# Kernel tuning notes

Measured on AMD Instinct MI355X. Metric: run time of the kernel, lower is better.

## Reference

```python
import jax, jax.numpy as jnp
import numpy as np

HEADS = 16
SEGS = 8


def _rotate_half(x):
    x1, x2 = jnp.split(x, 2, axis=-1)
    return jnp.concatenate([-x2, x1], axis=-1)


def _split_heads(t, h):
    b, n, dim = t.shape
    d = dim // h
    return t.reshape(b, n, h, d).transpose(0, 2, 1, 3).reshape(b * h, n, d)


def _merge_heads(t, b, h):
    c, n, d = t.shape
    return t.reshape(b, h, n, d).transpose(0, 2, 1, 3).reshape(b, n, h * d)


def setup_inputs() -> dict:
    key = jax.random.key(0)
    ks = jax.random.split(key, 5)
    b, n, dim = 2, 4096, 1024
    x = jax.random.normal(ks[0], (b, n, dim), dtype=jnp.float32)
    w = lambda k: jax.random.normal(k, (dim, dim), dtype=jnp.float32) * 0.02
    return {
        'x': x,
        'Wq': w(ks[1]),
        'Wkv': w(ks[2]),
        'Wo': w(ks[3]),
        'bo': jnp.zeros((dim,), jnp.float32),
        'Wo0': w(ks[4]),
        'bo0': jnp.zeros((dim,), jnp.float32),
    }


def reference(x, Wq, Wkv, Wo, bo, Wo0, bo0):
    b, n, dim = x.shape
    h = HEADS
    d = dim // h
    s = SEGS
    m = n // s  # segment_len
    mask_value = -jnp.finfo(x.dtype).max

    q = _split_heads(x @ Wq, h)    # (b*h, n, d)
    kv = _split_heads(x @ Wkv, h)  # (b*h, n, d)  (serves as both keys and values)

    # rotary embedding (layer_num == 0 branch)
    inv_freq = 1.0 / (10000.0 ** (jnp.arange(0, d, 2, dtype=jnp.float32) / d))
    freqs = jnp.arange(n, dtype=jnp.float32)[:, None] * inv_freq[None, :]  # (n, d/2)
    rot = jnp.concatenate([freqs, freqs], axis=-1)[None]  # (1, n, d)
    cos, sin = jnp.cos(rot), jnp.sin(rot)
    q = q * cos + _rotate_half(q) * sin
    kv = kv * cos + _rotate_half(kv) * sin

    q = q * (d ** -0.5)

    qs = q.reshape(-1, s, m, d)   # (c, s, m, d)
    kvs = kv.reshape(-1, s, m, d)

    # overlapping windows: segment t paired with segment t+1 as kv context
    kvs_ccs = jnp.concatenate([kvs[:, :-1], kvs[:, 1:]], axis=2)  # (c, s-1, 2m, d)
    qs_ccs = qs[:, 1:]                                            # (c, s-1, m, d)

    # NOTE: original computes lkv = LayerNorm(kvs_ccs) but never uses it (dead code) -> omitted.

    lsim = jnp.einsum('csmd,csnd->csmn', qs_ccs, kvs_ccs)  # (c, s-1, m, 2m)
    causal = jnp.triu(jnp.ones((m, m), dtype=bool), 1)
    # causal mask only applied to second half of keys (the own segment t+1)
    lsim = jnp.concatenate(
        [lsim[..., :m], jnp.where(causal, mask_value, lsim[..., m:])], axis=-1)

    attn0 = jnp.einsum('csmd,csnd->csmn', qs[:, :1], kvs[:, :1])  # (c, 1, m, m)
    attn0 = jnp.where(causal, mask_value, attn0)

    attn0 = jax.nn.softmax(attn0, axis=-1)
    attn1 = jax.nn.softmax(lsim, axis=-1)

    out0 = jnp.einsum('csij,csjd->csid', attn0, kvs[:, :1]).reshape(-1, m, d)
    out1 = jnp.einsum('csij,csjd->csid', attn1, kvs_ccs).reshape(-1, (s - 1) * m, d)

    out0 = _merge_heads(out0, b, h) @ Wo0 + bo0  # (b, m, dim)
    out1 = _merge_heads(out1, b, h) @ Wo + bo    # (b, (s-1)*m, dim)
    return jnp.concatenate([out0, out1], axis=1)  # (b, n, dim)
```

## Files before the change

kernel.cpp:

```cpp
#include <hip/hip_runtime.h>
#include <hip/hip_bf16.h>
#include <float.h>

using bf16 = __hip_bfloat16;
typedef __attribute__((ext_vector_type(8))) short bf16x8;
typedef __attribute__((ext_vector_type(4))) float f32x4;
typedef __attribute__((ext_vector_type(16))) float f32x16;

#define DIM   1024
#define NSEQ  4096
#define BATCH 2
#define NH    16
#define HD    64
#define NSEG  8
#define MSEG  512
#define ROWS  (BATCH*NSEQ)
#define NC    (BATCH*NH)
#define QSCALE (0.125f * 1.44269504f)

__device__ __forceinline__ float fast_exp2(float x) {
    float r;
    asm volatile("v_exp_f32 %0, %1" : "=v"(r) : "v"(x));
    return r;
}

__device__ __forceinline__ void gload16(const bf16* g, bf16* l) {
    __builtin_amdgcn_global_load_lds((const __attribute__((address_space(1))) unsigned int*)g,
                                     (__attribute__((address_space(3))) unsigned int*)l, 16, 0, 0);
}

__global__ void k_rope_tab(float* __restrict__ cosT, float* __restrict__ sinT) {
    int idx = blockIdx.x * 256 + threadIdx.x;
    int t = idx >> 5, i = idx & 31;
    float freq = 1.0f / powf(10000.0f, (float)(2 * i) * (1.0f / 64.0f));
    float a = (float)t * freq;
    cosT[idx] = cosf(a);
    sinT[idx] = sinf(a);
}

__global__ void k_convert_x(const float* __restrict__ X, bf16* __restrict__ Xb) {
    int i = (blockIdx.x * 256 + threadIdx.x) * 4;
    float4 v = *(const float4*)&X[i];
    union { bf16 h[4]; uint2 u; } p;
    p.h[0] = __float2bfloat16(v.x);
    p.h[1] = __float2bfloat16(v.y);
    p.h[2] = __float2bfloat16(v.z);
    p.h[3] = __float2bfloat16(v.w);
    *(uint2*)&Xb[i] = p.u;
}

__global__ void k_transpose(const float* __restrict__ W, bf16* __restrict__ Wt) {
    __shared__ float tile[32][33];
    int bx = blockIdx.x * 32;
    int by = blockIdx.y * 32;
    int tx = threadIdx.x;
    for (int i = threadIdx.y; i < 32; i += 8)
        tile[i][tx] = W[(size_t)(by + i) * DIM + bx + tx];
    __syncthreads();
    for (int i = threadIdx.y; i < 32; i += 8)
        Wt[(size_t)(bx + i) * DIM + by + tx] = __float2bfloat16(tile[tx][i]);
}

__launch_bounds__(256, 3)
__global__ void k_gemm_qkv(const bf16* __restrict__ A, const bf16* __restrict__ Bq,
                           const bf16* __restrict__ Bkv, const float* __restrict__ cosT,
                           const float* __restrict__ sinT, bf16* __restrict__ Qb,
                           bf16* __restrict__ KVf) {
    __shared__ alignas(16) bf16 SH[24576];
    bf16* AsB = SH;
    bf16* BsB = SH + 12288;
    const int K = DIM;
    int tid = threadIdx.x;
    int lane = tid & 63, wave = tid >> 6;
    int hi = lane >> 5, lq = lane & 31;
    int wr = (wave >> 1) * 64, wc = (wave & 1) * 64;
    int id = blockIdx.x;
    int xcd = id & 7, rank = id >> 3;
    int by = xcd * 8 + (rank >> 4);
    int bxx = rank & 15;
    int m0 = by * 128;
    bool isQ = (bxx < 8);
    const bf16* Bt = isQ ? Bq : Bkv;
    int n0 = (bxx & 7) * 128;
    int row = lane & 15, kk = (lane >> 4) * 8;
    int ch0 = wave * 128 + lane, ch1 = ch0 + 64;
    int r0 = ch0 >> 2, c0e = (ch0 & 3) * 8;
    int r1 = ch1 >> 2, c1e = (ch1 & 3) * 8;
    f32x4 acc[4][4] = {};

    auto stage = [&](int k0, int b) {
        gload16(&A[(size_t)(m0 + r0) * K + k0 + c0e], &AsB[b * 4096 + wave * 1024]);
        gload16(&A[(size_t)(m0 + r1) * K + k0 + c1e], &AsB[b * 4096 + wave * 1024 + 512]);
        gload16(&Bt[(size_t)(n0 + r0) * K + k0 + c0e], &BsB[b * 4096 + wave * 1024]);
        gload16(&Bt[(size_t)(n0 + r1) * K + k0 + c1e], &BsB[b * 4096 + wave * 1024 + 512]);
    };
    stage(0, 0);
    stage(32, 1);
    asm volatile("s_waitcnt vmcnt(4)" ::: "memory");
    __builtin_amdgcn_s_barrier();
    __builtin_amdgcn_sched_barrier(0);
    int cur = 0;
    for (int k = 0; k < 32; ++k) {
        if (k + 2 < 32) {
            int nb = cur + 2; if (nb >= 3) nb -= 3;
            stage(k * 32 + 64, nb);
        }
        bf16x8 af[4], bfr[4];
#pragma unroll
        for (int mt = 0; mt < 4; ++mt) af[mt] = *(const bf16x8*)&AsB[cur * 4096 + (wr + mt * 16 + row) * 32 + kk];
#pragma unroll
        for (int nt = 0; nt < 4; ++nt) bfr[nt] = *(const bf16x8*)&BsB[cur * 4096 + (wc + nt * 16 + row) * 32 + kk];
#pragma unroll
        for (int mt = 0; mt < 4; ++mt)
#pragma unroll
            for (int nt = 0; nt < 4; ++nt)
                acc[mt][nt] = __builtin_amdgcn_mfma_f32_16x16x32_bf16(af[mt], bfr[nt], acc[mt][nt], 0, 0, 0);
        if (k + 1 < 32) {
            if (k + 2 < 32) asm volatile("s_waitcnt vmcnt(4)" ::: "memory");
            else            asm volatile("s_waitcnt vmcnt(0)" ::: "memory");
            __builtin_amdgcn_s_barrier();
            __builtin_amdgcn_sched_barrier(0);
        }
        cur = cur + 1; if (cur == 3) cur = 0;
    }
    __syncthreads();
    bf16* Tw = SH + wave * (64 * 72);
    int orow = (lane >> 4) * 4, ocol = lane & 15;
    int head_g = (n0 + wc) >> 6;
    float sc = isQ ? QSCALE : 1.0f;
    int bidx = (m0 + wr) >> 12;
    int tbase = (m0 + wr) & (NSEQ - 1);
    int cch = bidx * NH + head_g;
#pragma unroll
    for (int mt = 0; mt < 4; ++mt) {
#pragma unroll
        for (int i = 0; i < 4; ++i) {
            int rl = mt * 16 + orow + i;
            int t = tbase + rl;
#pragma unroll
            for (int nt = 0; nt < 2; ++nt) {
                int e = nt * 16 + ocol;
                float x1 = acc[mt][nt][i], x2 = acc[mt][nt + 2][i];
                float cv = cosT[t * 32 + e], sv = sinT[t * 32 + e];
                Tw[rl * 72 + e]      = __float2bfloat16((x1 * cv - x2 * sv) * sc);
                Tw[rl * 72 + e + 32] = __float2bfloat16((x2 * cv + x1 * sv) * sc);
            }
        }
    }
    if (isQ) {
        int rsub = lane >> 3, dg = (lane & 7) * 8;
        size_t qbase = ((size_t)cch * NSEQ + tbase) * HD;
#pragma unroll
        for (int rr = 0; rr < 8; ++rr) {
            int rl = rr * 8 + rsub;
            *(uint4*)&Qb[qbase + (size_t)rl * HD + dg] = *(const uint4*)&Tw[rl * 72 + dg];
        }
    } else {
        size_t kvfbase = ((size_t)cch * 128 + (tbase >> 5)) * 4096;
#pragma unroll
        for (int st = 0; st < 2; ++st) {
            size_t tb = kvfbase + (size_t)st * 4096;
#pragma unroll
            for (int f = 0; f < 4; ++f)
                *(uint4*)&KVf[tb + f * 512 + lane * 8] =
                    *(const uint4*)&Tw[(st * 32 + lq) * 72 + f * 16 + hi * 8];
#pragma unroll
            for (int m = 0; m < 4; ++m) {
                int d0 = (m >> 1) * 32, sb = m & 1;
                union { bf16 h[8]; uint4 u; } pk;
#pragma unroll
                for (int j = 0; j < 8; ++j)
                    pk.h[j] = Tw[(st * 32 + sb * 16 + hi * 8 + j) * 72 + d0 + lq];
                *(uint4*)&KVf[tb + (size_t)(4 + m) * 512 + lane * 8] = pk.u;
            }
        }
    }
}

__launch_bounds__(256, 4)
__global__ void k_gemm_out(const bf16* __restrict__ A, const bf16* __restrict__ Bt0,
                           const bf16* __restrict__ Bt1, const float* __restrict__ bias0,
                           const float* __restrict__ bias1, float* __restrict__ C) {
    __shared__ alignas(16) bf16 As[3][128 * 32];
    __shared__ alignas(16) bf16 Bs[3][64 * 32];
    const int K = DIM;
    int tid = threadIdx.x;
    int lane = tid & 63, wave = tid >> 6;
    int wr = (wave >> 1) * 64, wc = (wave & 1) * 32;
    int id = blockIdx.x;
    int xcd = id & 7, rank = id >> 3;
    int by = xcd * 8 + (rank >> 4);
    int bx = rank & 15;
    int m0 = by * 128, n0 = bx * 64;
    bool first = (m0 & (NSEQ - 1)) < MSEG;
    const bf16* Bt = first ? Bt0 : Bt1;
    const float* bias = first ? bias0 : bias1;
    int row = lane & 15, kk = (lane >> 4) * 8;
    int ch0 = wave * 128 + lane, ch1 = ch0 + 64;
    int r0 = ch0 >> 2, c0e = (ch0 & 3) * 8;
    int r1 = ch1 >> 2, c1e = (ch1 & 3) * 8;
    int cb = wave * 64 + lane;
    int rb = cb >> 2, cbe = (cb & 3) * 8;
    f32x4 acc[4][2] = {};

    auto stage = [&](int k0, int b) {
        gload16(&A[(size_t)(m0 + r0) * K + k0 + c0e], &As[b][wave * 1024]);
        gload16(&A[(size_t)(m0 + r1) * K + k0 + c1e], &As[b][wave * 1024 + 512]);
        gload16(&Bt[(size_t)(n0 + rb) * K + k0 + cbe], &Bs[b][wave * 512]);
    };
    stage(0, 0);
    stage(32, 1);
    asm volatile("s_waitcnt vmcnt(3)" ::: "memory");
    __builtin_amdgcn_s_barrier();
    __builtin_amdgcn_sched_barrier(0);
    int cur = 0;
    for (int k = 0; k < 32; ++k) {
        if (k + 2 < 32) {
            int nb = cur + 2; if (nb >= 3) nb -= 3;
            stage(k * 32 + 64, nb);
        }
        bf16x8 af[4], bfr[2];
#pragma unroll
        for (int mt = 0; mt < 4; ++mt) af[mt] = *(const bf16x8*)&As[cur][(wr + mt * 16 + row) * 32 + kk];
#pragma unroll
        for (int nt = 0; nt < 2; ++nt) bfr[nt] = *(const bf16x8*)&Bs[cur][(wc + nt * 16 + row) * 32 + kk];
#pragma unroll
        for (int mt = 0; mt < 4; ++mt)
#pragma unroll
            for (int nt = 0; nt < 2; ++nt)
                acc[mt][nt] = __builtin_amdgcn_mfma_f32_16x16x32_bf16(af[mt], bfr[nt], acc[mt][nt], 0, 0, 0);
        if (k + 1 < 32) {
            if (k + 2 < 32) asm volatile("s_waitcnt vmcnt(3)" ::: "memory");
            else            asm volatile("s_waitcnt vmcnt(0)" ::: "memory");
            __builtin_amdgcn_s_barrier();
            __builtin_amdgcn_sched_barrier(0);
        }
        cur = cur + 1; if (cur == 3) cur = 0;
    }
    int orow = (lane >> 4) * 4, ocol = lane & 15;
#pragma unroll
    for (int mt = 0; mt < 4; ++mt)
#pragma unroll
        for (int nt = 0; nt < 2; ++nt) {
            float bv = bias[n0 + wc + nt * 16 + ocol];
#pragma unroll
            for (int i = 0; i < 4; ++i)
                C[(size_t)(m0 + wr + mt * 16 + orow + i) * DIM + n0 + wc + nt * 16 + ocol] = acc[mt][nt][i] + bv;
        }
}

__launch_bounds__(256, 4)
__global__ void k_attn(const bf16* __restrict__ Qb, const bf16* __restrict__ KVf,
                       bf16* __restrict__ Ob) {
    int lane = threadIdx.x & 63, wave = threadIdx.x >> 6;
    int hi = lane >> 5, lq = lane & 31;
    int id = blockIdx.x;
    int xcd = id & 7, rank = id >> 3;
    int c = xcd * 4 + (rank & 3);
    int hr = rank >> 2;
    int bx, seg;
    if (hr < 28) { bx = 3 - hr / 7; seg = 1 + hr % 7; }
    else         { seg = 0; bx = 31 - hr; }
    int i0 = bx * 128 + wave * 32;
    int bidx = c >> 4, head = c & 15;
    int tq = seg * MSEG + i0 + lq;
    const bf16* qptr = &Qb[((size_t)c * NSEQ + tq) * HD + hi * 8];
    bf16x8 qf[4];
#pragma unroll
    for (int dc = 0; dc < 4; ++dc) qf[dc] = *(const bf16x8*)&qptr[dc * 16];
    f32x16 o0 = {}, o1 = {};
    float mrun = -FLT_MAX, lrun = 0.f;
    int kvbase = (seg == 0) ? 0 : (seg - 1) * MSEG;
    int cstart = (seg == 0) ? 0 : MSEG;
    int cend = cstart + i0 + 32;
    int nT = cend >> 5;

    const bf16* fb = &KVf[((size_t)c * 128 + (kvbase >> 5)) * 4096 + lane * 8];

    bf16x8 ka0, ka1, ka2, ka3;
    f32x16 s;
    {
        bf16x8 k0 = *(const bf16x8*)&fb[0];
        bf16x8 k1 = *(const bf16x8*)&fb[512];
        bf16x8 k2 = *(const bf16x8*)&fb[1024];
        bf16x8 k3 = *(const bf16x8*)&fb[1536];
        if (nT > 1) {
            const bf16* p1 = fb + 4096;
            ka0 = *(const bf16x8*)&p1[0];
            ka1 = *(const bf16x8*)&p1[512];
            ka2 = *(const bf16x8*)&p1[1024];
            ka3 = *(const bf16x8*)&p1[1536];
        }
        f32x16 z = {};
        __builtin_amdgcn_s_setprio(1);
        z = __builtin_amdgcn_mfma_f32_32x32x16_bf16(k0, qf[0], z, 0, 0, 0);
        z = __builtin_amdgcn_mfma_f32_32x32x16_bf16(k1, qf[1], z, 0, 0, 0);
        z = __builtin_amdgcn_mfma_f32_32x32x16_bf16(k2, qf[2], z, 0, 0, 0);
        z = __builtin_amdgcn_mfma_f32_32x32x16_bf16(k3, qf[3], z, 0, 0, 0);
        __builtin_amdgcn_s_setprio(0);
        s = z;
    }

    for (int it = 0; it < nT; ++it) {
        int c0 = it * 32;
        const bf16* pv = fb + (size_t)it * 4096 + 2048;
        bf16x8 vf0 = *(const bf16x8*)&pv[0];
        bf16x8 vf1 = *(const bf16x8*)&pv[512];
        bf16x8 vf2 = *(const bf16x8*)&pv[1024];
        bf16x8 vf3 = *(const bf16x8*)&pv[1536];
        if (c0 + 31 >= cstart && c0 + 31 - cstart > i0) {
#pragma unroll
            for (int r = 0; r < 16; ++r) {
                int kvg = c0 + ((r & 3) + 8 * (r >> 2) + 4 * hi);
                if (kvg >= cstart && kvg - cstart > i0 + lq) s[r] = -FLT_MAX;
            }
        }
        float m8[8], m4[4];
#pragma unroll
        for (int r = 0; r < 8; ++r) m8[r] = fmaxf(s[2 * r], s[2 * r + 1]);
#pragma unroll
        for (int r = 0; r < 4; ++r) m4[r] = fmaxf(m8[2 * r], m8[2 * r + 1]);
        float vmax = fmaxf(fmaxf(m4[0], m4[1]), fmaxf(m4[2], m4[3]));
        vmax = fmaxf(vmax, __shfl_xor(vmax, 32));
        if (__any(vmax > mrun + 11.5f)) {
            float nm = fmaxf(mrun, vmax);
            float al = fast_exp2(mrun - nm);
#pragma unroll
            for (int r = 0; r < 16; ++r) { o0[r] *= al; o1[r] *= al; }
            lrun *= al;
            mrun = nm;
        }
        float p[16];
#pragma unroll
        for (int r = 0; r < 16; ++r) p[r] = fast_exp2(s[r] - mrun);
        if (it + 1 < nT) {
            f32x16 z = {};
            __builtin_amdgcn_s_setprio(1);
            z = __builtin_amdgcn_mfma_f32_32x32x16_bf16(ka0, qf[0], z, 0, 0, 0);
            z = __builtin_amdgcn_mfma_f32_32x32x16_bf16(ka1, qf[1], z, 0, 0, 0);
            z = __builtin_amdgcn_mfma_f32_32x32x16_bf16(ka2, qf[2], z, 0, 0, 0);
            z = __builtin_amdgcn_mfma_f32_32x32x16_bf16(ka3, qf[3], z, 0, 0, 0);
            __builtin_amdgcn_s_setprio(0);
            s = z;
            if (it + 2 < nT) {
                const bf16* pn = fb + (size_t)(it + 2) * 4096;
                ka0 = *(const bf16x8*)&pn[0];
                ka1 = *(const bf16x8*)&pn[512];
                ka2 = *(const bf16x8*)&pn[1024];
                ka3 = *(const bf16x8*)&pn[1536];
            }
        }
        float a8[8], a4[4];
#pragma unroll
        for (int r = 0; r < 8; ++r) a8[r] = p[2 * r] + p[2 * r + 1];
#pragma unroll
        for (int r = 0; r < 4; ++r) a4[r] = a8[2 * r] + a8[2 * r + 1];
        lrun += (a4[0] + a4[1]) + (a4[2] + a4[3]);
        unsigned pk[8];
#pragma unroll
        for (int k = 0; k < 8; ++k) {
            union { bf16 h[2]; unsigned u; } cv;
            cv.h[0] = __float2bfloat16(p[2 * k]);
            cv.h[1] = __float2bfloat16(p[2 * k + 1]);
            pk[k] = cv.u;
        }
        unsigned u0 = hi ? pk[0] : pk[2];
        unsigned u1 = hi ? pk[1] : pk[3];
        unsigned u2 = hi ? pk[4] : pk[6];
        unsigned u3 = hi ? pk[5] : pk[7];
        unsigned w0 = (unsigned)__shfl_xor((int)u0, 32);
        unsigned w1 = (unsigned)__shfl_xor((int)u1, 32);
        unsigned w2 = (unsigned)__shfl_xor((int)u2, 32);
        unsigned w3 = (unsigned)__shfl_xor((int)u3, 32);
        union { unsigned u[4]; bf16x8 v; } b0, b1;
        b0.u[0] = hi ? w0 : pk[0];
        b0.u[1] = hi ? w1 : pk[1];
        b0.u[2] = hi ? pk[2] : w0;
        b0.u[3] = hi ? pk[3] : w1;
        b1.u[0] = hi ? w2 : pk[4];
        b1.u[1] = hi ? w3 : pk[5];
        b1.u[2] = hi ? pk[6] : w2;
        b1.u[3] = hi ? pk[7] : w3;
        __builtin_amdgcn_s_setprio(1);
        o0 = __builtin_amdgcn_mfma_f32_32x32x16_bf16(vf0, b0.v, o0, 0, 0, 0);
        o1 = __builtin_amdgcn_mfma_f32_32x32x16_bf16(vf2, b0.v, o1, 0, 0, 0);
        o0 = __builtin_amdgcn_mfma_f32_32x32x16_bf16(vf1, b1.v, o0, 0, 0, 0);
        o1 = __builtin_amdgcn_mfma_f32_32x32x16_bf16(vf3, b1.v, o1, 0, 0, 0);
        __builtin_amdgcn_s_setprio(0);
    }
    lrun += __shfl_xor(lrun, 32);
    float inv = 1.0f / lrun;
    size_t obase = ((size_t)bidx * NSEQ + tq) * DIM + head * HD;
#pragma unroll
    for (int dt = 0; dt < 2; ++dt)
#pragma unroll
        for (int a = 0; a < 4; ++a) {
            union { bf16 h[4]; uint2 u; } pkd;
            const f32x16& ov = dt ? o1 : o0;
#pragma unroll
            for (int i = 0; i < 4; ++i) pkd.h[i] = __float2bfloat16(ov[4 * a + i] * inv);
            *(uint2*)&Ob[obase + dt * 32 + 8 * a + 4 * hi] = pkd.u;
        }
}

extern "C" void kernel_launch(void* const* d_in, const int* in_sizes, int n_in,
                              void* d_out, int out_size, void* d_ws, size_t ws_size,
                              hipStream_t stream) {
    const float* x   = (const float*)d_in[0];
    const float* Wq  = (const float*)d_in[1];
    const float* Wkv = (const float*)d_in[2];
    const float* Wo  = (const float*)d_in[3];
    const float* bo  = (const float*)d_in[4];
    const float* Wo0 = (const float*)d_in[5];
    const float* bo0 = (const float*)d_in[6];
    float* out = (float*)d_out;

    char* ws = (char*)d_ws;
    size_t off = 0;
    auto alloc = [&](size_t bytes) { void* p = ws + off; off += (bytes + 255) & ~(size_t)255; return p; };
    float* cosT = (float*)alloc((size_t)NSEQ * 32 * 4);
    float* sinT = (float*)alloc((size_t)NSEQ * 32 * 4);
    bf16* Xb    = (bf16*)alloc((size_t)ROWS * DIM * 2);
    bf16* WqT   = (bf16*)alloc((size_t)DIM * DIM * 2);
    bf16* WkvT  = (bf16*)alloc((size_t)DIM * DIM * 2);
    bf16* WoT   = (bf16*)alloc((size_t)DIM * DIM * 2);
    bf16* Wo0T  = (bf16*)alloc((size_t)DIM * DIM * 2);
    bf16* Qb    = (bf16*)alloc((size_t)NC * NSEQ * HD * 2);
    bf16* KVf   = (bf16*)alloc((size_t)NC * 128 * 4096 * 2);
    bf16* Ob    = (bf16*)alloc((size_t)ROWS * DIM * 2);

    hipLaunchKernelGGL(k_rope_tab, dim3(NSEQ * 32 / 256), dim3(256), 0, stream, cosT, sinT);
    hipLaunchKernelGGL(k_convert_x, dim3(ROWS * DIM / 4 / 256), dim3(256), 0, stream, x, Xb);
    hipLaunchKernelGGL(k_transpose, dim3(32, 32), dim3(32, 8), 0, stream, Wq, WqT);
    hipLaunchKernelGGL(k_transpose, dim3(32, 32), dim3(32, 8), 0, stream, Wkv, WkvT);
    hipLaunchKernelGGL(k_transpose, dim3(32, 32), dim3(32, 8), 0, stream, Wo, WoT);
    hipLaunchKernelGGL(k_transpose, dim3(32, 32), dim3(32, 8), 0, stream, Wo0, Wo0T);

    hipLaunchKernelGGL(k_gemm_qkv, dim3(1024), dim3(256), 0, stream, Xb, WqT, WkvT, cosT, sinT, Qb, KVf);

    hipLaunchKernelGGL(k_attn, dim3(1024), dim3(256), 0, stream, Qb, KVf, Ob);

    hipLaunchKernelGGL(k_gemm_out, dim3(1024), dim3(256), 0, stream, Ob, Wo0T, WoT, bo0, bo, out);
}
```

Measured before the change: 154.5 us.

## Merge prep kernels into one launch and XOR-swizzle GEMM LDS tiles

Six small preprocessing launches (rope table, x conversion, four weight transposes) become one kernel that picks its task from the block index, which removes launch gaps. Both GEMM kernels now XOR-swizzle the 8-element k-chunk column by row bits, both when staging global data into LDS and when reading MFMA fragments, to reduce LDS bank conflicts. The swizzle moves the permutation onto the global-load addresses, so each lane reads a permuted 16-byte chunk within its row.

New measurement: 142.6 us. -7.7%, faster.

```diff
diff --git a/kernel.cpp b/kernel.cpp
--- a/kernel.cpp
+++ b/kernel.cpp
@@ -29,36 +29,43 @@
                                      (__attribute__((address_space(3))) unsigned int*)l, 16, 0, 0);
 }
 
-__global__ void k_rope_tab(float* __restrict__ cosT, float* __restrict__ sinT) {
-    int idx = blockIdx.x * 256 + threadIdx.x;
-    int t = idx >> 5, i = idx & 31;
-    float freq = 1.0f / powf(10000.0f, (float)(2 * i) * (1.0f / 64.0f));
-    float a = (float)t * freq;
-    cosT[idx] = cosf(a);
-    sinT[idx] = sinf(a);
-}
-
-__global__ void k_convert_x(const float* __restrict__ X, bf16* __restrict__ Xb) {
-    int i = (blockIdx.x * 256 + threadIdx.x) * 4;
-    float4 v = *(const float4*)&X[i];
-    union { bf16 h[4]; uint2 u; } p;
-    p.h[0] = __float2bfloat16(v.x);
-    p.h[1] = __float2bfloat16(v.y);
-    p.h[2] = __float2bfloat16(v.z);
-    p.h[3] = __float2bfloat16(v.w);
-    *(uint2*)&Xb[i] = p.u;
-}
-
-__global__ void k_transpose(const float* __restrict__ W, bf16* __restrict__ Wt) {
+__global__ void k_prep(const float* __restrict__ x, bf16* __restrict__ Xb,
+                       const float* __restrict__ Wq, const float* __restrict__ Wkv,
+                       const float* __restrict__ Wo, const float* __restrict__ Wo0,
+                       bf16* __restrict__ WqT, bf16* __restrict__ WkvT,
+                       bf16* __restrict__ WoT, bf16* __restrict__ Wo0T,
+                       float* __restrict__ cosT, float* __restrict__ sinT) {
     __shared__ float tile[32][33];
-    int bx = blockIdx.x * 32;
-    int by = blockIdx.y * 32;
-    int tx = threadIdx.x;
-    for (int i = threadIdx.y; i < 32; i += 8)
-        tile[i][tx] = W[(size_t)(by + i) * DIM + bx + tx];
-    __syncthreads();
-    for (int i = threadIdx.y; i < 32; i += 8)
-        Wt[(size_t)(bx + i) * DIM + by + tx] = __float2bfloat16(tile[tx][i]);
+    int b = blockIdx.x, tid = threadIdx.x;
+    if (b < 8192) {
+        int i = (b * 256 + tid) * 4;
+        float4 v = *(const float4*)&x[i];
+        union { bf16 h[4]; uint2 u; } p;
+        p.h[0] = __float2bfloat16(v.x);
+        p.h[1] = __float2bfloat16(v.y);
+        p.h[2] = __float2bfloat16(v.z);
+        p.h[3] = __float2bfloat16(v.w);
+        *(uint2*)&Xb[i] = p.u;
+    } else if (b < 12288) {
+        int zz = (b - 8192) >> 10;
+        int bb = (b - 8192) & 1023;
+        int bxt = (bb & 31) * 32, byt = (bb >> 5) * 32;
+        const float* W = (zz == 0) ? Wq : (zz == 1) ? Wkv : (zz == 2) ? Wo : Wo0;
+        bf16* Wt = (zz == 0) ? WqT : (zz == 1) ? WkvT : (zz == 2) ? WoT : Wo0T;
+        int tx = tid & 31, ty = tid >> 5;
+        for (int ii = ty; ii < 32; ii += 8)
+            tile[ii][tx] = W[(size_t)(byt + ii) * DIM + bxt + tx];
+        __syncthreads();
+        for (int ii = ty; ii < 32; ii += 8)
+            Wt[(size_t)(bxt + ii) * DIM + byt + tx] = __float2bfloat16(tile[tx][ii]);
+    } else {
+        int idx = (b - 12288) * 256 + tid;
+        int t = idx >> 5, ii = idx & 31;
+        float freq = 1.0f / powf(10000.0f, (float)(2 * ii) * (1.0f / 64.0f));
+        float a = (float)t * freq;
+        cosT[idx] = cosf(a);
+        sinT[idx] = sinf(a);
+    }
 }
 
 __launch_bounds__(256, 3)
@@ -83,16 +90,19 @@
     const bf16* Bt = isQ ? Bq : Bkv;
     int n0 = (bxx & 7) * 128;
     int row = lane & 15, kk = (lane >> 4) * 8;
+    int kkA = kk ^ (((lane >> 1) & 3) << 3);
     int ch0 = wave * 128 + lane, ch1 = ch0 + 64;
     int r0 = ch0 >> 2, c0e = (ch0 & 3) * 8;
     int r1 = ch1 >> 2, c1e = (ch1 & 3) * 8;
+    int c0s = c0e ^ (((r0 >> 1) & 3) << 3);
+    int c1s = c1e ^ (((r1 >> 1) & 3) << 3);
     f32x4 acc[4][4] = {};
 
     auto stage = [&](int k0, int b) {
-        gload16(&A[(size_t)(m0 + r0) * K + k0 + c0e], &AsB[b * 4096 + wave * 1024]);
-        gload16(&A[(size_t)(m0 + r1) * K + k0 + c1e], &AsB[b * 4096 + wave * 1024 + 512]);
-        gload16(&Bt[(size_t)(n0 + r0) * K + k0 + c0e], &BsB[b * 4096 + wave * 1024]);
-        gload16(&Bt[(size_t)(n0 + r1) * K + k0 + c1e], &BsB[b * 4096 + wave * 1024 + 512]);
+        gload16(&A[(size_t)(m0 + r0) * K + k0 + c0s], &AsB[b * 4096 + wave * 1024]);
+        gload16(&A[(size_t)(m0 + r1) * K + k0 + c1s], &AsB[b * 4096 + wave * 1024 + 512]);
+        gload16(&Bt[(size_t)(n0 + r0) * K + k0 + c0s], &BsB[b * 4096 + wave * 1024]);
+        gload16(&Bt[(size_t)(n0 + r1) * K + k0 + c1s], &BsB[b * 4096 + wave * 1024 + 512]);
     };
     stage(0, 0);
     stage(32, 1);
@@ -107,9 +117,9 @@
         }
         bf16x8 af[4], bfr[4];
 #pragma unroll
-        for (int mt = 0; mt < 4; ++mt) af[mt] = *(const bf16x8*)&AsB[cur * 4096 + (wr + mt * 16 + row) * 32 + kk];
-#pragma unroll
-        for (int nt = 0; nt < 4; ++nt) bfr[nt] = *(const bf16x8*)&BsB[cur * 4096 + (wc + nt * 16 + row) * 32 + kk];
+        for (int mt = 0; mt < 4; ++mt) af[mt] = *(const bf16x8*)&AsB[cur * 4096 + (wr + mt * 16 + row) * 32 + kkA];
+#pragma unroll
+        for (int nt = 0; nt < 4; ++nt) bfr[nt] = *(const bf16x8*)&BsB[cur * 4096 + (wc + nt * 16 + row) * 32 + kkA];
 #pragma unroll
         for (int mt = 0; mt < 4; ++mt)
 #pragma unroll
@@ -196,17 +206,21 @@
     const bf16* Bt = first ? Bt0 : Bt1;
     const float* bias = first ? bias0 : bias1;
     int row = lane & 15, kk = (lane >> 4) * 8;
+    int kkA = kk ^ (((lane >> 1) & 3) << 3);
     int ch0 = wave * 128 + lane, ch1 = ch0 + 64;
     int r0 = ch0 >> 2, c0e = (ch0 & 3) * 8;
     int r1 = ch1 >> 2, c1e = (ch1 & 3) * 8;
+    int c0s = c0e ^ (((r0 >> 1) & 3) << 3);
+    int c1s = c1e ^ (((r1 >> 1) & 3) << 3);
     int cb = wave * 64 + lane;
     int rb = cb >> 2, cbe = (cb & 3) * 8;
+    int cbs = cbe ^ (((rb >> 1) & 3) << 3);
     f32x4 acc[4][2] = {};
 
     auto stage = [&](int k0, int b) {
-        gload16(&A[(size_t)(m0 + r0) * K + k0 + c0e], &As[b][wave * 1024]);
-        gload16(&A[(size_t)(m0 + r1) * K + k0 + c1e], &As[b][wave * 1024 + 512]);
-        gload16(&Bt[(size_t)(n0 + rb) * K + k0 + cbe], &Bs[b][wave * 512]);
+        gload16(&A[(size_t)(m0 + r0) * K + k0 + c0s], &As[b][wave * 1024]);
+        gload16(&A[(size_t)(m0 + r1) * K + k0 + c1s], &As[b][wave * 1024 + 512]);
+        gload16(&Bt[(size_t)(n0 + rb) * K + k0 + cbs], &Bs[b][wave * 512]);
     };
     stage(0, 0);
     stage(32, 1);
@@ -221,9 +235,9 @@
         }
         bf16x8 af[4], bfr[2];
 #pragma unroll
-        for (int mt = 0; mt < 4; ++mt) af[mt] = *(const bf16x8*)&As[cur][(wr + mt * 16 + row) * 32 + kk];
-#pragma unroll
-        for (int nt = 0; nt < 2; ++nt) bfr[nt] = *(const bf16x8*)&Bs[cur][(wc + nt * 16 + row) * 32 + kk];
+        for (int mt = 0; mt < 4; ++mt) af[mt] = *(const bf16x8*)&As[cur][(wr + mt * 16 + row) * 32 + kkA];
+#pragma unroll
+        for (int nt = 0; nt < 2; ++nt) bfr[nt] = *(const bf16x8*)&Bs[cur][(wc + nt * 16 + row) * 32 + kkA];
 #pragma unroll
         for (int mt = 0; mt < 4; ++mt)
 #pragma unroll
@@ -429,12 +443,8 @@
     bf16* KVf   = (bf16*)alloc((size_t)NC * 128 * 4096 * 2);
     bf16* Ob    = (bf16*)alloc((size_t)ROWS * DIM * 2);
 
-    hipLaunchKernelGGL(k_rope_tab, dim3(NSEQ * 32 / 256), dim3(256), 0, stream, cosT, sinT);
-    hipLaunchKernelGGL(k_convert_x, dim3(ROWS * DIM / 4 / 256), dim3(256), 0, stream, x, Xb);
-    hipLaunchKernelGGL(k_transpose, dim3(32, 32), dim3(32, 8), 0, stream, Wq, WqT);
-    hipLaunchKernelGGL(k_transpose, dim3(32, 32), dim3(32, 8), 0, stream, Wkv, WkvT);
-    hipLaunchKernelGGL(k_transpose, dim3(32, 32), dim3(32, 8), 0, stream, Wo, WoT);
-    hipLaunchKernelGGL(k_transpose, dim3(32, 32), dim3(32, 8), 0, stream, Wo0, Wo0T);
+    hipLaunchKernelGGL(k_prep, dim3(12800), dim3(256), 0, stream,
+                       x, Xb, Wq, Wkv, Wo, Wo0, WqT, WkvT, WoT, Wo0T, cosT, sinT);
 
     hipLaunchKernelGGL(k_gemm_qkv, dim3(1024), dim3(256), 0, stream, Xb, WqT, WkvT, cosT, sinT, Qb, KVf);
 
```
